# Kernel tuning notes

Measured on AMD Instinct MI355X. Metric: run time of the kernel, lower is better.

The kernel has to match this reference:

```python
import jax, jax.numpy as jnp
from jax import lax
import numpy as np

NUM_LAYERS = 6
KERNEL = 3
FILTERS = 64
STENCIL = 4
IN_CH = 3  # C, vx, vy
SHIFT = 0.0
VAR = 1.0


def periodic_conv(x, w, b):
    # x: [B,H,W,Cin], w: [k,k,Cin,Cout] -> periodic ('wrap') padding + VALID conv
    p = w.shape[0] // 2
    xp = jnp.pad(x, ((0, 0), (p, p), (p, p), (0, 0)), mode='wrap')
    y = lax.conv_general_dilated(xp, w, (1, 1), 'VALID',
                                 dimension_numbers=('NHWC', 'HWIO', 'NHWC'))
    return y + b


def stencil_shift_tensors(c, size):
    # c: [B,H,W] -> [B,H,W,size*size] of periodically rolled copies
    half = size // 2
    shifts = [jnp.roll(c, shift=(half - i, half - j), axis=(1, 2))
              for i in range(size) for j in range(size)]
    return jnp.stack(shifts, axis=-1)


def setup_inputs() -> dict:
    key = jax.random.key(0)
    ks = jax.random.split(key, 16)
    B, H, W = 8, 256, 256
    inp = {
        'C': jax.random.normal(ks[0], (B, H, W), jnp.float32),
        'vx': jax.random.normal(ks[1], (B, H, W), jnp.float32),
        'vy': jax.random.normal(ks[2], (B, H, W), jnp.float32),
    }
    fan_in0 = KERNEL * KERNEL * IN_CH
    inp['w0'] = jax.random.normal(ks[3], (KERNEL, KERNEL, IN_CH, FILTERS), jnp.float32) / np.sqrt(fan_in0)
    inp['b0'] = jnp.zeros((FILTERS,), jnp.float32)
    fan_in = KERNEL * KERNEL * FILTERS
    for i in range(1, NUM_LAYERS - 1):
        inp[f'w{i}'] = jax.random.normal(ks[3 + i], (KERNEL, KERNEL, FILTERS, FILTERS), jnp.float32) / np.sqrt(fan_in)
        inp[f'b{i}'] = jnp.zeros((FILTERS,), jnp.float32)
    inp['wout'] = jax.random.normal(ks[10], (KERNEL, KERNEL, FILTERS, STENCIL * STENCIL), jnp.float32) / np.sqrt(fan_in)
    inp['bout'] = jnp.zeros((STENCIL * STENCIL,), jnp.float32)
    return inp


def reference(C, vx, vy, w0, b0, w1, b1, w2, b2, w3, b3, w4, b4, wout, bout):
    ws = [w0, w1, w2, w3, w4]
    bs = [b0, b1, b2, b3, b4]
    x = jnp.stack([(C - SHIFT) / VAR, vx, vy], axis=-1)  # [B,H,W,3]
    for w, b in zip(ws, bs):
        x = jax.nn.relu(periodic_conv(x, w, b))
    coeffs = periodic_conv(x, wout, bout)  # [B,H,W,S^2]
    stencil = stencil_shift_tensors(C, STENCIL)  # [B,H,W,S^2]
    # einsum 'ijkl,ijkl->ijk'
    return jnp.einsum('bhws,bhws->bhw', coeffs, stencil)
```

## Files before the change

### kernel.cpp

```cpp
#include <hip/hip_runtime.h>
#include <hip/hip_bf16.h>


#define HW   256
#define MASK 255
#define CH   64
#define TX   32
#define TY   16

typedef short bf16x8 __attribute__((ext_vector_type(8)));
typedef float f32x4  __attribute__((ext_vector_type(4)));

__device__ __forceinline__ float bf2f(unsigned short u) {
    return __uint_as_float(((unsigned int)u) << 16);
}
__device__ __forceinline__ unsigned short f2bf(float f) {
    unsigned int x = __float_as_uint(f);
    return (unsigned short)((x + 0x7fffu + ((x >> 16) & 1u)) >> 16);
}

__global__ __launch_bounds__(512) void k_pack(
    const float* __restrict__ w1, const float* __restrict__ w2,
    const float* __restrict__ w3, const float* __restrict__ w4,
    unsigned short* __restrict__ dst)
{
    int g = blockIdx.x * 512 + threadIdx.x;
    if (g >= 4 * 4608) return;
    int L = g / 4608, r = g - L * 4608;
    const float* w = (L == 0) ? w1 : (L == 1) ? w2 : (L == 2) ? w3 : w4;
    int q = r >> 8, n = (r >> 6) & 3, l = r & 63;
    int tap = q >> 1, s = q & 1;
    int ci0 = s * 32 + ((l >> 4) << 3);
    int co  = n * 16 + (l & 15);
    unsigned short o8[8];
#pragma unroll
    for (int j = 0; j < 8; j++)
        o8[j] = f2bf(w[(tap * 64 + ci0 + j) * 64 + co]);
    *reinterpret_cast<uint4*>(dst + (size_t)g * 8) = *reinterpret_cast<uint4*>(o8);
}

__global__ __launch_bounds__(512) void k_layer0(
    const float* __restrict__ Cin, const float* __restrict__ vx,
    const float* __restrict__ vy, const float* __restrict__ w0,
    const float* __restrict__ b0, unsigned short* __restrict__ out)
{
    int t  = threadIdx.x;
    int lx = t & 31, ly = t >> 5;
    int x  = blockIdx.x * TX + lx;
    int y  = blockIdx.y * TY + ly;
    int bb = blockIdx.z;
    int pbase = bb * HW * HW;

    float a[27];
#pragma unroll
    for (int ky = 0; ky < 3; ky++) {
        int yy = (y + ky - 1) & MASK;
#pragma unroll
        for (int kx = 0; kx < 3; kx++) {
            int xx  = (x + kx - 1) & MASK;
            int idx = pbase + yy * HW + xx;
            a[(ky * 3 + kx) * 3 + 0] = Cin[idx];
            a[(ky * 3 + kx) * 3 + 1] = vx[idx];
            a[(ky * 3 + kx) * 3 + 2] = vy[idx];
        }
    }

    size_t obase = ((size_t)(pbase + y * HW + x)) * CH;
    for (int c4 = 0; c4 < 4; c4++) {
        float acc[16];
#pragma unroll
        for (int j = 0; j < 16; j++) acc[j] = b0[c4 * 16 + j];
#pragma unroll
        for (int k = 0; k < 27; k++) {
            float av = a[k];
            const float* wq = w0 + k * CH + c4 * 16;
#pragma unroll
            for (int j = 0; j < 16; j++) acc[j] = fmaf(av, wq[j], acc[j]);
        }
        unsigned short o[16];
#pragma unroll
        for (int j = 0; j < 16; j++) o[j] = f2bf(fmaxf(acc[j], 0.f));
        *reinterpret_cast<uint4*>(out + obase + c4 * 16)     = *reinterpret_cast<uint4*>(o);
        *reinterpret_cast<uint4*>(out + obase + c4 * 16 + 8) = *reinterpret_cast<uint4*>(o + 8);
    }
}

__global__ __launch_bounds__(512, 4) void k_mid_v5(
    const unsigned short* __restrict__ in,
    const unsigned short* __restrict__ wp,
    const float* __restrict__ b, unsigned short* __restrict__ out)
{
    __shared__ unsigned short sAct[18 * 34 * CH];

    const int t    = threadIdx.x;
    const int lane = t & 63;
    const int wid  = t >> 6;
    const int l15  = lane & 15;
    const int l4   = lane >> 4;

    const int bid = blockIdx.x;
    const int tid = (bid & 7) * 128 + (bid >> 3);
    const int bz  = tid >> 7;
    const int rr  = tid & 127;
    const int y0  = (rr >> 3) * 16;
    const int x0  = (rr & 7) * 32;
    const size_t pbase = (size_t)bz * HW * HW;

    for (int g = t; g < 18 * 34 * 8; g += 512) {
        int hp = g >> 3, cg = g & 7;
        int hr = hp / 34, hc = hp - hr * 34;
        int gy = (y0 + hr - 1) & MASK;
        int gx = (x0 + hc - 1) & MASK;
        uint4 v = *reinterpret_cast<const uint4*>(
            in + ((pbase + gy * HW + gx) * CH + cg * 8));
        *reinterpret_cast<uint4*>(&sAct[hp * 64 + ((cg ^ (hp & 7)) << 3)]) = v;
    }

    bf16x8 bnx[4];
#pragma unroll
    for (int n = 0; n < 4; n++)
        bnx[n] = *reinterpret_cast<const bf16x8*>(wp + (size_t)(n * 512 + lane * 8));

    __syncthreads();

    f32x4 acc[4][4];
#pragma unroll
    for (int m = 0; m < 4; m++)
#pragma unroll
        for (int n = 0; n < 4; n++) {
            float bv = b[n * 16 + l15];
            acc[m][n] = (f32x4){bv, bv, bv, bv};
        }

    int pxb[4];
#pragma unroll
    for (int m = 0; m < 4; m++)
        pxb[m] = (2 * wid + (m >> 1)) * 34 + (m & 1) * 16 + l15;

#pragma unroll
    for (int tap = 0; tap < 9; tap++) {
        const int koff = (tap / 3) * 34 + (tap % 3);
#pragma unroll
        for (int s = 0; s < 2; s++) {
            const int q = tap * 2 + s;
            bf16x8 bc[4];
#pragma unroll
            for (int n = 0; n < 4; n++) bc[n] = bnx[n];
            if (q < 17) {
#pragma unroll
                for (int n = 0; n < 4; n++)
                    bnx[n] = *reinterpret_cast<const bf16x8*>(
                        wp + (size_t)(((q + 1) * 4 + n) * 512 + lane * 8));
            }
            const int o = s * 4 + l4;
#pragma unroll
            for (int m = 0; m < 4; m++) {
                int px  = pxb[m] + koff;
                int off = (px << 6) + (((o ^ px) & 7) << 3);
                bf16x8 af = *reinterpret_cast<const bf16x8*>(&sAct[off]);
#pragma unroll
                for (int n = 0; n < 4; n++)
                    acc[m][n] = __builtin_amdgcn_mfma_f32_16x16x32_bf16(
                        af, bc[n], acc[m][n], 0, 0, 0);
            }
        }
    }

#pragma unroll
    for (int m = 0; m < 4; m++) {
        int y = y0 + 2 * wid + (m >> 1);
        int x = x0 + (m & 1) * 16;
        unsigned short* pm = out + (pbase + (size_t)y * HW + x) * CH + (l4 << 8) + l15;
#pragma unroll
        for (int n = 0; n < 4; n++)
#pragma unroll
            for (int j = 0; j < 4; j++)
                pm[j * 64 + n * 16] = f2bf(fmaxf(acc[m][n][j], 0.f));
    }
}

__global__ __launch_bounds__(512, 2) void k_out_mfma(
    const unsigned short* __restrict__ in, const float* __restrict__ w,
    const float* __restrict__ b, const float* __restrict__ Cin,
    float* __restrict__ out)
{
    __shared__ unsigned short sAct[18 * 34 * CH];
    __shared__ unsigned short sW[9 * 128 * 8];
    __shared__ float sC[19 * 35];

    const int t    = threadIdx.x;
    const int lane = t & 63;
    const int wid  = t >> 6;
    const int l15  = lane & 15;
    const int l4   = lane >> 4;
    const int x0   = blockIdx.x * 32;
    const int y0   = blockIdx.y * 16;
    const size_t pbase = (size_t)blockIdx.z * HW * HW;

    for (int g = t; g < 18 * 34 * 8; g += 512) {
        int hp = g >> 3, cg = g & 7;
        int hr = hp / 34, hc = hp - hr * 34;
        int gy = (y0 + hr - 1) & MASK;
        int gx = (x0 + hc - 1) & MASK;
        uint4 v = *reinterpret_cast<const uint4*>(
            in + ((pbase + gy * HW + gx) * CH + cg * 8));
        *reinterpret_cast<uint4*>(&sAct[hp * 64 + ((cg ^ (hp & 7)) << 3)]) = v;
    }
    for (int g = t; g < 1152; g += 512) {
        int tap = g >> 7, s = (g >> 6) & 1, dl = g & 63;
        int ci0 = s * 32 + (dl >> 4) * 8;
        int co  = dl & 15;
        unsigned short o8[8];
#pragma unroll
        for (int j = 0; j < 8; j++)
            o8[j] = f2bf(w[(tap * 64 + ci0 + j) * 16 + co]);
        *reinterpret_cast<uint4*>(&sW[g * 8]) = *reinterpret_cast<uint4*>(o8);
    }
    for (int g = t; g < 19 * 35; g += 512) {
        int r = g / 35, c2 = g - r * 35;
        int gy = (y0 + r - 2) & MASK;
        int gx = (x0 + c2 - 2) & MASK;
        sC[g] = Cin[pbase + gy * HW + gx];
    }
    __syncthreads();

    f32x4 acc[4];
    {
        float bv = b[l15];
#pragma unroll
        for (int m = 0; m < 4; m++) acc[m] = (f32x4){bv, bv, bv, bv};
    }

    int pxb[4];
#pragma unroll
    for (int m = 0; m < 4; m++)
        pxb[m] = (2 * wid + (m >> 1)) * 34 + (m & 1) * 16 + l15;

    for (int tap = 0; tap < 9; tap++) {
        const int koff = (tap / 3) * 34 + (tap % 3);
#pragma unroll
        for (int s = 0; s < 2; s++) {
            bf16x8 bf = *reinterpret_cast<const bf16x8*>(
                &sW[((tap * 2 + s) << 9) + (lane << 3)]);
            const int o = s * 4 + l4;
#pragma unroll
            for (int m = 0; m < 4; m++) {
                int px  = pxb[m] + koff;
                int off = (px << 6) + (((o ^ px) & 7) << 3);
                bf16x8 af = *reinterpret_cast<const bf16x8*>(&sAct[off]);
                acc[m] = __builtin_amdgcn_mfma_f32_16x16x32_bf16(
                    af, bf, acc[m], 0, 0, 0);
            }
        }
    }

#pragma unroll
    for (int m = 0; m < 4; m++) {
        int py = 2 * wid + (m >> 1);
        int xb = (m & 1) * 16 + l4 * 4;
#pragma unroll
        for (int j = 0; j < 4; j++) {
            int xt = xb + j;
            float v = acc[m][j] * sC[(py + (l15 >> 2)) * 35 + xt + (l15 & 3)];
            v += __shfl_xor(v, 1);
            v += __shfl_xor(v, 2);
            v += __shfl_xor(v, 4);
            v += __shfl_xor(v, 8);
            if (l15 == 0)
                out[pbase + (y0 + py) * HW + x0 + xt] = v;
        }
    }
}

extern "C" void kernel_launch(void* const* d_in, const int* in_sizes, int n_in,
                              void* d_out, int out_size, void* d_ws, size_t ws_size,
                              hipStream_t stream)
{
    (void)in_sizes; (void)n_in; (void)out_size; (void)ws_size;
    const float* Cin  = (const float*)d_in[0];
    const float* vx   = (const float*)d_in[1];
    const float* vy   = (const float*)d_in[2];
    const float* w0   = (const float*)d_in[3];
    const float* b0   = (const float*)d_in[4];
    const float* w1   = (const float*)d_in[5];
    const float* b1   = (const float*)d_in[6];
    const float* w2   = (const float*)d_in[7];
    const float* b2   = (const float*)d_in[8];
    const float* w3   = (const float*)d_in[9];
    const float* b3   = (const float*)d_in[10];
    const float* w4   = (const float*)d_in[11];
    const float* b4   = (const float*)d_in[12];
    const float* wout = (const float*)d_in[13];
    const float* bout = (const float*)d_in[14];

    unsigned short* actA = (unsigned short*)d_ws;
    unsigned short* actB = actA + (size_t)8 * HW * HW * CH;

    unsigned short* wpk = (unsigned short*)d_out;

    dim3 block(512);
    dim3 grid0(HW / TX, HW / TY, 8);
    dim3 gridM(1024);
    dim3 gridO(HW / 32, HW / 16, 8);

    k_pack    <<<36, block, 0, stream>>>(w1, w2, w3, w4, wpk);
    k_layer0  <<<grid0, block, 0, stream>>>(Cin, vx, vy, w0, b0, actA);
    k_mid_v5  <<<gridM, block, 0, stream>>>(actA, wpk + 0 * 36864, b1, actB);
    k_mid_v5  <<<gridM, block, 0, stream>>>(actB, wpk + 1 * 36864, b2, actA);
    k_mid_v5  <<<gridM, block, 0, stream>>>(actA, wpk + 2 * 36864, b3, actB);
    k_mid_v5  <<<gridM, block, 0, stream>>>(actB, wpk + 3 * 36864, b4, actA);
    k_out_mfma<<<gridO, block, 0, stream>>>(actA, wout, bout, Cin, (float*)d_out);
}
```

Measured before the change: 254.5 us.

## Make mid conv kernel persistent over four tiles with double-buffered LDS prefetch

```diff
diff --git a/kernel.cpp b/kernel.cpp
--- a/kernel.cpp
+++ b/kernel.cpp
@@ -85,12 +85,12 @@
     }
 }
 
-__global__ __launch_bounds__(512, 4) void k_mid_v5(
+__global__ __launch_bounds__(512, 2) void k_mid_v10(
     const unsigned short* __restrict__ in,
     const unsigned short* __restrict__ wp,
     const float* __restrict__ b, unsigned short* __restrict__ out)
 {
-    __shared__ unsigned short sAct[18 * 34 * CH];
+    __shared__ unsigned short sA[2][18 * 34 * CH];
 
     const int t    = threadIdx.x;
     const int lane = t & 63;
@@ -98,22 +98,21 @@
     const int l15  = lane & 15;
     const int l4   = lane >> 4;
 
-    const int bid = blockIdx.x;
-    const int tid = (bid & 7) * 128 + (bid >> 3);
-    const int bz  = tid >> 7;
-    const int rr  = tid & 127;
-    const int y0  = (rr >> 3) * 16;
-    const int x0  = (rr & 7) * 32;
-    const size_t pbase = (size_t)bz * HW * HW;
-
-    for (int g = t; g < 18 * 34 * 8; g += 512) {
-        int hp = g >> 3, cg = g & 7;
-        int hr = hp / 34, hc = hp - hr * 34;
-        int gy = (y0 + hr - 1) & MASK;
-        int gx = (x0 + hc - 1) & MASK;
-        uint4 v = *reinterpret_cast<const uint4*>(
-            in + ((pbase + gy * HW + gx) * CH + cg * 8));
-        *reinterpret_cast<uint4*>(&sAct[hp * 64 + ((cg ^ (hp & 7)) << 3)]) = v;
+    const int tb = blockIdx.x * 4;
+
+    {
+        const int bz = tb >> 7, rr = tb & 127;
+        const int y0 = (rr >> 3) * 16, x0 = (rr & 7) * 32;
+        const size_t pbase = (size_t)bz * HW * HW;
+        for (int g = t; g < 4896; g += 512) {
+            int hp = g >> 3, cg = g & 7;
+            int hr = hp / 34, hc = hp - hr * 34;
+            int gy = (y0 + hr - 1) & MASK;
+            int gx = (x0 + hc - 1) & MASK;
+            uint4 v = *reinterpret_cast<const uint4*>(
+                in + ((pbase + (size_t)gy * HW + gx) * CH + cg * 8));
+            *reinterpret_cast<uint4*>(&sA[0][hp * 64 + ((cg ^ (hp & 7)) << 3)]) = v;
+        }
     }
 
     bf16x8 bnx[4];
@@ -123,59 +122,105 @@
 
     __syncthreads();
 
-    f32x4 acc[4][4];
-#pragma unroll
-    for (int m = 0; m < 4; m++)
-#pragma unroll
-        for (int n = 0; n < 4; n++) {
-            float bv = b[n * 16 + l15];
-            acc[m][n] = (f32x4){bv, bv, bv, bv};
-        }
-
     int pxb[4];
 #pragma unroll
     for (int m = 0; m < 4; m++)
         pxb[m] = (2 * wid + (m >> 1)) * 34 + (m & 1) * 16 + l15;
 
-#pragma unroll
-    for (int tap = 0; tap < 9; tap++) {
-        const int koff = (tap / 3) * 34 + (tap % 3);
-#pragma unroll
-        for (int s = 0; s < 2; s++) {
-            const int q = tap * 2 + s;
-            bf16x8 bc[4];
-#pragma unroll
-            for (int n = 0; n < 4; n++) bc[n] = bnx[n];
-            if (q < 17) {
-#pragma unroll
-                for (int n = 0; n < 4; n++)
-                    bnx[n] = *reinterpret_cast<const bf16x8*>(
-                        wp + (size_t)(((q + 1) * 4 + n) * 512 + lane * 8));
-            }
-            const int o = s * 4 + l4;
-#pragma unroll
-            for (int m = 0; m < 4; m++) {
-                int px  = pxb[m] + koff;
-                int off = (px << 6) + (((o ^ px) & 7) << 3);
-                bf16x8 af = *reinterpret_cast<const bf16x8*>(&sAct[off]);
-#pragma unroll
-                for (int n = 0; n < 4; n++)
-                    acc[m][n] = __builtin_amdgcn_mfma_f32_16x16x32_bf16(
-                        af, bc[n], acc[m][n], 0, 0, 0);
-            }
-        }
-    }
-
-#pragma unroll
-    for (int m = 0; m < 4; m++) {
-        int y = y0 + 2 * wid + (m >> 1);
-        int x = x0 + (m & 1) * 16;
-        unsigned short* pm = out + (pbase + (size_t)y * HW + x) * CH + (l4 << 8) + l15;
-#pragma unroll
-        for (int n = 0; n < 4; n++)
-#pragma unroll
-            for (int j = 0; j < 4; j++)
-                pm[j * 64 + n * 16] = f2bf(fmaxf(acc[m][n][j], 0.f));
+    for (int it = 0; it < 4; ++it) {
+        const int tid = tb + it;
+        const int bz = tid >> 7, rr = tid & 127;
+        const int y0 = (rr >> 3) * 16, x0 = (rr & 7) * 32;
+        const size_t pbase = (size_t)bz * HW * HW;
+        const unsigned short* sbuf = &sA[it & 1][0];
+
+        uint4 st[10];
+        {
+            const int ntid = (tid + 1) & 1023;
+            const int nbz = ntid >> 7, nrr = ntid & 127;
+            const int ny0 = (nrr >> 3) * 16, nx0 = (nrr & 7) * 32;
+            const size_t npb = (size_t)nbz * HW * HW;
+#pragma unroll
+            for (int i2 = 0; i2 < 10; ++i2) {
+                int gg = i2 * 512 + t; if (gg >= 4896) gg -= 4896;
+                int hp = gg >> 3, cg = gg & 7;
+                int hr = hp / 34, hc = hp - hr * 34;
+                int gy = (ny0 + hr - 1) & MASK;
+                int gx = (nx0 + hc - 1) & MASK;
+                st[i2] = *reinterpret_cast<const uint4*>(
+                    in + ((npb + (size_t)gy * HW + gx) * CH + cg * 8));
+            }
+        }
+
+        f32x4 acc[4][4];
+#pragma unroll
+        for (int m = 0; m < 4; m++)
+#pragma unroll
+            for (int n = 0; n < 4; n++) {
+                float bv = b[n * 16 + l15];
+                acc[m][n] = (f32x4){bv, bv, bv, bv};
+            }
+
+#pragma unroll
+        for (int tap = 0; tap < 9; tap++) {
+            const int koff = (tap / 3) * 34 + (tap % 3);
+#pragma unroll
+            for (int s = 0; s < 2; s++) {
+                const int q = tap * 2 + s;
+                bf16x8 bc[4];
+#pragma unroll
+                for (int n = 0; n < 4; n++) bc[n] = bnx[n];
+                if (q < 17) {
+#pragma unroll
+                    for (int n = 0; n < 4; n++)
+                        bnx[n] = *reinterpret_cast<const bf16x8*>(
+                            wp + (size_t)(((q + 1) * 4 + n) * 512 + lane * 8));
+                }
+                const int o = s * 4 + l4;
+#pragma unroll
+                for (int m = 0; m < 4; m++) {
+                    int px  = pxb[m] + koff;
+                    int off = (px << 6) + (((o ^ px) & 7) << 3);
+                    bf16x8 af = *reinterpret_cast<const bf16x8*>(&sbuf[off]);
+#pragma unroll
+                    for (int n = 0; n < 4; n++)
+                        acc[m][n] = __builtin_amdgcn_mfma_f32_16x16x32_bf16(
+                            af, bc[n], acc[m][n], 0, 0, 0);
+                }
+            }
+        }
+
+        if (it < 3) {
+            unsigned short* dbuf = &sA[(it + 1) & 1][0];
+#pragma unroll
+            for (int i2 = 0; i2 < 10; ++i2) {
+                int gg = i2 * 512 + t; if (gg >= 4896) gg -= 4896;
+                int hp = gg >> 3, cg = gg & 7;
+                *reinterpret_cast<uint4*>(
+                    &dbuf[hp * 64 + ((cg ^ (hp & 7)) << 3)]) = st[i2];
+            }
+        }
+        __syncthreads();
+
+#pragma unroll
+        for (int m = 0; m < 4; m++) {
+            int y = y0 + 2 * wid + (m >> 1);
+            int x = x0 + (m & 1) * 16;
+            unsigned short* pm =
+                out + (pbase + (size_t)y * HW + x) * CH + (l4 << 8) + l15;
+#pragma unroll
+            for (int n = 0; n < 4; n++)
+#pragma unroll
+                for (int j = 0; j < 4; j++)
+                    pm[j * 64 + n * 16] = f2bf(fmaxf(acc[m][n][j], 0.f));
+        }
+
+        if (it < 3) {
+#pragma unroll
+            for (int n = 0; n < 4; n++)
+                bnx[n] = *reinterpret_cast<const bf16x8*>(
+                    wp + (size_t)(n * 512 + lane * 8));
+        }
     }
 }
 
@@ -300,14 +345,14 @@
 
     dim3 block(512);
     dim3 grid0(HW / TX, HW / TY, 8);
-    dim3 gridM(1024);
+    dim3 gridM(256);
     dim3 gridO(HW / 32, HW / 16, 8);
 
     k_pack    <<<36, block, 0, stream>>>(w1, w2, w3, w4, wpk);
     k_layer0  <<<grid0, block, 0, stream>>>(Cin, vx, vy, w0, b0, actA);
-    k_mid_v5  <<<gridM, block, 0, stream>>>(actA, wpk + 0 * 36864, b1, actB);
-    k_mid_v5  <<<gridM, block, 0, stream>>>(actB, wpk + 1 * 36864, b2, actA);
-    k_mid_v5  <<<gridM, block, 0, stream>>>(actA, wpk + 2 * 36864, b3, actB);
-    k_mid_v5  <<<gridM, block, 0, stream>>>(actB, wpk + 3 * 36864, b4, actA);
+    k_mid_v10 <<<gridM, block, 0, stream>>>(actA, wpk + 0 * 36864, b1, actB);
+    k_mid_v10 <<<gridM, block, 0, stream>>>(actB, wpk + 1 * 36864, b2, actA);
+    k_mid_v10 <<<gridM, block, 0, stream>>>(actA, wpk + 2 * 36864, b3, actB);
+    k_mid_v10 <<<gridM, block, 0, stream>>>(actB, wpk + 3 * 36864, b4, actA);
     k_out_mfma<<<gridO, block, 0, stream>>>(actA, wout, bout, Cin, (float*)d_out);
 }
```

New measurement: 996.3 us. +291.4%, slower.
